# Optimization experiments

Measured on AMD Instinct MI355X. Metric: run time of the kernel, lower is better.

The kernel has to match this reference:

```python
import jax, jax.numpy as jnp
import numpy as np

D_MODEL = 512
N_HEADS = 8
D_HEAD = D_MODEL // N_HEADS


def setup_inputs() -> dict:
    key = jax.random.key(0)
    ks = jax.random.split(key, 10)
    B, N = 4, 2048
    s = 1.0 / np.sqrt(D_MODEL)
    inp = {
        'x': jax.random.normal(ks[0], (B, N, D_MODEL), jnp.float32),
        'attn_bias': jax.random.normal(ks[1], (B, 1, N, N), jnp.float32),
        'wq': jax.random.normal(ks[2], (D_MODEL, D_MODEL), jnp.float32) * s,
        'bq': jnp.zeros((D_MODEL,), jnp.float32),
        'wk': jax.random.normal(ks[3], (D_MODEL, D_MODEL), jnp.float32) * s,
        'bk': jnp.zeros((D_MODEL,), jnp.float32),
        'wv': jax.random.normal(ks[4], (D_MODEL, D_MODEL), jnp.float32) * s,
        'bv': jnp.zeros((D_MODEL,), jnp.float32),
        'wo': jax.random.normal(ks[5], (D_MODEL, D_MODEL), jnp.float32) * s,
        'bo': jnp.zeros((D_MODEL,), jnp.float32),
    }
    return inp


def reference(x, attn_bias, wq, bq, wk, bk, wv, bv, wo, bo):
    B, N, D = x.shape
    h, dh = N_HEADS, D_HEAD
    # projections; weights stored as (in, out) so y = x @ w + b
    q = (x @ wq + bq).reshape(B, N, h, dh).transpose(0, 2, 1, 3)  # (B,h,N,dh)
    k = (x @ wk + bk).reshape(B, N, h, dh).transpose(0, 2, 1, 3)
    v = (x @ wv + bv).reshape(B, N, h, dh).transpose(0, 2, 1, 3)
    scores = jnp.einsum('bhnd,bhmd->bhnm', q, k) / jnp.sqrt(jnp.float32(dh))
    scores = scores + attn_bias  # broadcast over heads
    attn = jax.nn.softmax(scores, axis=-1)
    out = jnp.einsum('bhnm,bhmd->bhnd', attn, v)
    out = out.transpose(0, 2, 1, 3).reshape(B, N, D)
    return out @ wo + bo
```

## Files before the change

### kernel.cpp

```cpp
#include <hip/hip_runtime.h>
#include <hip/hip_bf16.h>

typedef __bf16 bf16x8 __attribute__((ext_vector_type(8)));
typedef float f32x4 __attribute__((ext_vector_type(4)));
using u16 = unsigned short;
using u32 = unsigned int;

#define LDSS 72

__device__ __forceinline__ u16 f2bf(float f) {
  union { float f; u32 u; } v; v.f = f;
  u32 r = v.u + 0x7fffu + ((v.u >> 16) & 1u);
  return (u16)(r >> 16);
}

__device__ __forceinline__ u32 cvt_pk_bf16(float lo, float hi) {
  u32 r;
  asm("v_cvt_pk_bf16_f32 %0, %1, %2" : "=v"(r) : "v"(lo), "v"(hi));
  return r;
}

__global__ void cast_x_kernel(const float* __restrict__ x, u16* __restrict__ xb) {
  int i = (blockIdx.x * 256 + threadIdx.x) * 8;
  float4 f0 = *(const float4*)&x[i];
  float4 f1 = *(const float4*)&x[i + 4];
  u16 u[8];
  u[0] = f2bf(f0.x); u[1] = f2bf(f0.y); u[2] = f2bf(f0.z); u[3] = f2bf(f0.w);
  u[4] = f2bf(f1.x); u[5] = f2bf(f1.y); u[6] = f2bf(f1.z); u[7] = f2bf(f1.w);
  *(uint4*)&xb[i] = *(uint4*)u;
}

__global__ void cast_wT_kernel(const float* __restrict__ w0, const float* __restrict__ w1,
                               const float* __restrict__ w2, const float* __restrict__ w3,
                               u16* __restrict__ t0, u16* __restrict__ t1,
                               u16* __restrict__ t2, u16* __restrict__ t3) {
  int i = blockIdx.x * 256 + threadIdx.x;
  int wi = i >> 18;
  int r = i & 262143;
  int row = r >> 9, col = r & 511;
  const float* w; u16* t;
  if (wi == 0)      { w = w0; t = t0; }
  else if (wi == 1) { w = w1; t = t1; }
  else if (wi == 2) { w = w2; t = t2; }
  else              { w = w3; t = t3; }
  t[col * 512 + row] = f2bf(w[r]);
}

__global__ __launch_bounds__(256) void proj_kernel(
    const u16* __restrict__ xb,
    const u16* __restrict__ wqT, const u16* __restrict__ wkT, const u16* __restrict__ wvT,
    const float* __restrict__ bq, const float* __restrict__ bk, const float* __restrict__ bv,
    u16* __restrict__ Q, u16* __restrict__ K, u16* __restrict__ Vt) {
  __shared__ u16 Alds[64 * LDSS];
  __shared__ u16 Blds[64 * LDSS];
  int which = blockIdx.z;
  const u16* wT; const float* bias; u16* out;
  if (which == 0)      { wT = wqT; bias = bq; out = Q; }
  else if (which == 1) { wT = wkT; bias = bk; out = K; }
  else                 { wT = wvT; bias = bv; out = Vt; }

  int m0 = blockIdx.y * 64;
  int n0 = blockIdx.x * 64;
  int tid = threadIdx.x;
  int lane = tid & 63, w = tid >> 6;
  int wm = w >> 1, wn = w & 1;
  int l15 = lane & 15, l4 = lane >> 4;

  f32x4 acc[2][2] = {};
  for (int k0 = 0; k0 < 512; k0 += 64) {
    __syncthreads();
#pragma unroll
    for (int c = tid; c < 512; c += 256) {
      int row = c >> 3, c8 = (c & 7) * 8;
      *(uint4*)&Alds[row * LDSS + c8] = *(const uint4*)&xb[(m0 + row) * 512 + k0 + c8];
      *(uint4*)&Blds[row * LDSS + c8] = *(const uint4*)&wT[(n0 + row) * 512 + k0 + c8];
    }
    __syncthreads();
#pragma unroll
    for (int kk = 0; kk < 2; kk++) {
      bf16x8 a[2], b[2];
#pragma unroll
      for (int f = 0; f < 2; f++) {
        a[f] = *(const bf16x8*)&Alds[(wm * 32 + f * 16 + l15) * LDSS + kk * 32 + l4 * 8];
        b[f] = *(const bf16x8*)&Blds[(wn * 32 + f * 16 + l15) * LDSS + kk * 32 + l4 * 8];
      }
#pragma unroll
      for (int fm = 0; fm < 2; fm++)
#pragma unroll
        for (int fn = 0; fn < 2; fn++) {
          if (which == 2)
            acc[fm][fn] = __builtin_amdgcn_mfma_f32_16x16x32_bf16(b[fn], a[fm], acc[fm][fn], 0, 0, 0);
          else
            acc[fm][fn] = __builtin_amdgcn_mfma_f32_16x16x32_bf16(a[fm], b[fn], acc[fm][fn], 0, 0, 0);
        }
    }
  }
  int bidx = m0 >> 11;
  int head = n0 >> 6;
  if (which == 2) {
#pragma unroll
    for (int fm = 0; fm < 2; fm++)
#pragma unroll
      for (int fn = 0; fn < 2; fn++)
#pragma unroll
        for (int r = 0; r < 4; r++) {
          int drow = wn * 32 + fn * 16 + l4 * 4 + r;
          int col  = wm * 32 + fm * 16 + l15;
          float vv = acc[fm][fn][r] + bias[n0 + drow];
          out[((size_t)(bidx * 8 + head) * 64 + drow) * 2048 + (m0 & 2047) + col] = f2bf(vv);
        }
  } else {
#pragma unroll
    for (int fm = 0; fm < 2; fm++)
#pragma unroll
      for (int fn = 0; fn < 2; fn++)
#pragma unroll
        for (int r = 0; r < 4; r++) {
          int row = wm * 32 + fm * 16 + l4 * 4 + r;
          int col = wn * 32 + fn * 16 + l15;
          int nrow = (m0 & 2047) + row;
          float vv = acc[fm][fn][r] + bias[n0 + col];
          out[(((size_t)(bidx * 8 + head) * 2048) + nrow) * 64 + col] = f2bf(vv);
        }
  }
}

__global__ __launch_bounds__(512, 4) void attn_kernel(
    const u16* __restrict__ Q, const u16* __restrict__ K, const u16* __restrict__ Vt,
    const float* __restrict__ bias, u16* __restrict__ O) {
  __shared__ u16 Klds[64 * LDSS];
  __shared__ u16 Vtlds[64 * LDSS];

  int qt = blockIdx.x, h = blockIdx.y, b = blockIdx.z;
  int tid = threadIdx.x;
  int lane = tid & 63, w = tid >> 6;
  int l15 = lane & 15, l4 = lane >> 4;
  int qrow = qt * 128 + w * 16 + l15;

  const u16* Qbh  = Q  + (size_t)(b * 8 + h) * 2048 * 64;
  const u16* Kbh  = K  + (size_t)(b * 8 + h) * 2048 * 64;
  const u16* Vtbh = Vt + (size_t)(b * 8 + h) * 64 * 2048;
  const float* biasrow = bias + (size_t)b * 2048 * 2048 + (size_t)qrow * 2048;

  bf16x8 aq[2];
#pragma unroll
  for (int kk = 0; kk < 2; kk++)
    aq[kk] = *(const bf16x8*)&Qbh[qrow * 64 + kk * 32 + l4 * 8];

  f32x4 o[4] = {};
  float mrow = -1e30f, lrow = 0.f;

  int srcA = (lane & 16) * 2 + l15;
  bool hiF = (l4 >> 1) != 0;

  int srow = tid >> 3, sc8 = (tid & 7) * 8;

  uint4 kr = *(const uint4*)&Kbh[srow * 64 + sc8];
  uint4 vr = *(const uint4*)&Vtbh[srow * 2048 + sc8];
  float4 bb[4];
#pragma unroll
  for (int fj = 0; fj < 4; fj++)
    bb[fj] = *(const float4*)&biasrow[fj * 16 + l4 * 4];

  for (int t = 0; t < 32; t++) {
    __syncthreads();
    *(uint4*)&Klds[srow * LDSS + sc8]  = kr;
    *(uint4*)&Vtlds[srow * LDSS + sc8] = vr;
    __syncthreads();

    bool pf = (t < 31);
    float4 nbb[4];
    if (pf) {
      kr = *(const uint4*)&Kbh[((t + 1) * 64 + srow) * 64 + sc8];
      vr = *(const uint4*)&Vtbh[srow * 2048 + (t + 1) * 64 + sc8];
#pragma unroll
      for (int fj = 0; fj < 4; fj++)
        nbb[fj] = *(const float4*)&biasrow[(t + 1) * 64 + fj * 16 + l4 * 4];
    }

    f32x4 s[4] = {};
#pragma unroll
    for (int kk = 0; kk < 2; kk++)
#pragma unroll
      for (int fj = 0; fj < 4; fj++) {
        bf16x8 kf = *(const bf16x8*)&Klds[(fj * 16 + l15) * LDSS + kk * 32 + l4 * 8];
        s[fj] = __builtin_amdgcn_mfma_f32_16x16x32_bf16(kf, aq[kk], s[fj], 0, 0, 0);
      }

    float m = -1e30f;
#pragma unroll
    for (int fj = 0; fj < 4; fj++)
#pragma unroll
      for (int r = 0; r < 4; r++) {
        s[fj][r] = s[fj][r] * 0.125f + ((const float*)&bb[fj])[r];
        m = fmaxf(m, s[fj][r]);
      }
    m = fmaxf(m, __shfl_xor(m, 16));
    m = fmaxf(m, __shfl_xor(m, 32));
    float mnew = fmaxf(mrow, m);
    float corr = __expf(mrow - mnew);
    mrow = mnew;

    u32 pk[4][2];
    float sum = 0.f;
#pragma unroll
    for (int fj = 0; fj < 4; fj++) {
      float p0 = __expf(s[fj][0] - mnew);
      float p1 = __expf(s[fj][1] - mnew);
      float p2 = __expf(s[fj][2] - mnew);
      float p3 = __expf(s[fj][3] - mnew);
      sum += (p0 + p1) + (p2 + p3);
      pk[fj][0] = cvt_pk_bf16(p0, p1);
      pk[fj][1] = cvt_pk_bf16(p2, p3);
    }
    sum += __shfl_xor(sum, 16);
    sum += __shfl_xor(sum, 32);
    lrow = lrow * corr + sum;
#pragma unroll
    for (int fo = 0; fo < 4; fo++)
#pragma unroll
      for (int r = 0; r < 4; r++) o[fo][r] *= corr;

#pragma unroll
    for (int kk = 0; kk < 2; kk++) {
      u32 a0 = __shfl((int)pk[2 * kk][0],     srcA);
      u32 b0 = __shfl((int)pk[2 * kk + 1][0], srcA);
      u32 a1 = __shfl((int)pk[2 * kk][1],     srcA);
      u32 b1 = __shfl((int)pk[2 * kk + 1][1], srcA);
      u32 a2 = __shfl((int)pk[2 * kk][0],     srcA + 16);
      u32 b2 = __shfl((int)pk[2 * kk + 1][0], srcA + 16);
      u32 a3 = __shfl((int)pk[2 * kk][1],     srcA + 16);
      u32 b3 = __shfl((int)pk[2 * kk + 1][1], srcA + 16);
      union { u32 u[4]; bf16x8 v; } pu;
      pu.u[0] = hiF ? b0 : a0;
      pu.u[1] = hiF ? b1 : a1;
      pu.u[2] = hiF ? b2 : a2;
      pu.u[3] = hiF ? b3 : a3;
#pragma unroll
      for (int fo = 0; fo < 4; fo++) {
        bf16x8 vt = *(const bf16x8*)&Vtlds[(fo * 16 + l15) * LDSS + kk * 32 + l4 * 8];
        o[fo] = __builtin_amdgcn_mfma_f32_16x16x32_bf16(vt, pu.v, o[fo], 0, 0, 0);
      }
    }

    if (pf) {
#pragma unroll
      for (int fj = 0; fj < 4; fj++) bb[fj] = nbb[fj];
    }
  }

  float inv = 1.0f / lrow;
  size_t obase = (size_t)(b * 2048 + qrow) * 512 + h * 64;
#pragma unroll
  for (int fo = 0; fo < 4; fo++) {
    u32 wlo = cvt_pk_bf16(o[fo][0] * inv, o[fo][1] * inv);
    u32 whi = cvt_pk_bf16(o[fo][2] * inv, o[fo][3] * inv);
    *(u32*)&O[obase + fo * 16 + l4 * 4]     = wlo;
    *(u32*)&O[obase + fo * 16 + l4 * 4 + 2] = whi;
  }
}

__global__ __launch_bounds__(256) void outproj_kernel(
    const u16* __restrict__ Ob, const u16* __restrict__ woT,
    const float* __restrict__ bo, float* __restrict__ out) {
  __shared__ u16 Alds[64 * LDSS];
  __shared__ u16 Blds[64 * LDSS];
  int m0 = blockIdx.y * 64;
  int n0 = blockIdx.x * 64;
  int tid = threadIdx.x;
  int lane = tid & 63, w = tid >> 6;
  int wm = w >> 1, wn = w & 1;
  int l15 = lane & 15, l4 = lane >> 4;

  f32x4 acc[2][2] = {};
  for (int k0 = 0; k0 < 512; k0 += 64) {
    __syncthreads();
#pragma unroll
    for (int c = tid; c < 512; c += 256) {
      int row = c >> 3, c8 = (c & 7) * 8;
      *(uint4*)&Alds[row * LDSS + c8] = *(const uint4*)&Ob[(m0 + row) * 512 + k0 + c8];
      *(uint4*)&Blds[row * LDSS + c8] = *(const uint4*)&woT[(n0 + row) * 512 + k0 + c8];
    }
    __syncthreads();
#pragma unroll
    for (int kk = 0; kk < 2; kk++) {
      bf16x8 a[2], bfr[2];
#pragma unroll
      for (int f = 0; f < 2; f++) {
        a[f] = *(const bf16x8*)&Alds[(wm * 32 + f * 16 + l15) * LDSS + kk * 32 + l4 * 8];
        bfr[f] = *(const bf16x8*)&Blds[(wn * 32 + f * 16 + l15) * LDSS + kk * 32 + l4 * 8];
      }
#pragma unroll
      for (int fm = 0; fm < 2; fm++)
#pragma unroll
        for (int fn = 0; fn < 2; fn++)
          acc[fm][fn] = __builtin_amdgcn_mfma_f32_16x16x32_bf16(a[fm], bfr[fn], acc[fm][fn], 0, 0, 0);
    }
  }
#pragma unroll
  for (int fm = 0; fm < 2; fm++)
#pragma unroll
    for (int fn = 0; fn < 2; fn++)
#pragma unroll
      for (int r = 0; r < 4; r++) {
        int row = wm * 32 + fm * 16 + l4 * 4 + r;
        int col = wn * 32 + fn * 16 + l15;
        out[(size_t)(m0 + row) * 512 + n0 + col] = acc[fm][fn][r] + bo[n0 + col];
      }
}

extern "C" void kernel_launch(void* const* d_in, const int* in_sizes, int n_in,
                              void* d_out, int out_size, void* d_ws, size_t ws_size,
                              hipStream_t stream) {
  const float* x    = (const float*)d_in[0];
  const float* bias = (const float*)d_in[1];
  const float* wq   = (const float*)d_in[2];
  const float* bq   = (const float*)d_in[3];
  const float* wk   = (const float*)d_in[4];
  const float* bk   = (const float*)d_in[5];
  const float* wv   = (const float*)d_in[6];
  const float* bv   = (const float*)d_in[7];
  const float* wo   = (const float*)d_in[8];
  const float* bo   = (const float*)d_in[9];
  float* out = (float*)d_out;

  char* ws = (char*)d_ws;
  u16* xb  = (u16*)(ws + 0);
  u16* wqT = (u16*)(ws + 8388608);
  u16* wkT = (u16*)(ws + 8912896);
  u16* wvT = (u16*)(ws + 9437184);
  u16* woT = (u16*)(ws + 9961472);
  u16* Qb  = (u16*)(ws + 10485760);
  u16* Kb  = (u16*)(ws + 18874368);
  u16* VtB = (u16*)(ws + 27262976);
  u16* Ob  = (u16*)(ws + 35651584);

  hipLaunchKernelGGL(cast_x_kernel, dim3(2048), dim3(256), 0, stream, x, xb);
  hipLaunchKernelGGL(cast_wT_kernel, dim3(4096), dim3(256), 0, stream,
                     wq, wk, wv, wo, wqT, wkT, wvT, woT);
  hipLaunchKernelGGL(proj_kernel, dim3(8, 128, 3), dim3(256), 0, stream,
                     xb, wqT, wkT, wvT, bq, bk, bv, Qb, Kb, VtB);
  hipLaunchKernelGGL(attn_kernel, dim3(16, 8, 4), dim3(512), 0, stream,
                     Qb, Kb, VtB, bias, Ob);
  hipLaunchKernelGGL(outproj_kernel, dim3(8, 128), dim3(256), 0, stream,
                     Ob, woT, bo, out);
}
```

Measured before the change: 154.3 us.

## Prefetch GEMM tiles in registers, shrink attention blocks, add lazy rescale and setprio

The projection and output-projection GEMMs now load the next K-slice into registers while computing on the current LDS tile, which overlaps global loads with MFMA work. The attention kernel moves from 512-thread blocks covering 128 query rows to 256-thread blocks covering 64 rows, doubling the grid. It also adds s_setprio around the MFMA sections and skips the online-softmax rescale unless the running max grows by more than 8. The lazy rescale saves exp and multiply work per tile, but lets unnormalised exponentials reach up to e^8 before correction.

```diff
diff --git a/kernel.cpp b/kernel.cpp
--- a/kernel.cpp
+++ b/kernel.cpp
@@ -66,16 +66,28 @@
   int wm = w >> 1, wn = w & 1;
   int l15 = lane & 15, l4 = lane >> 4;
 
+  int r0 = tid >> 3, c8 = (tid & 7) * 8;
+
+  uint4 ar0 = *(const uint4*)&xb[(m0 + r0) * 512 + c8];
+  uint4 ar1 = *(const uint4*)&xb[(m0 + r0 + 32) * 512 + c8];
+  uint4 br0 = *(const uint4*)&wT[(n0 + r0) * 512 + c8];
+  uint4 br1 = *(const uint4*)&wT[(n0 + r0 + 32) * 512 + c8];
+
   f32x4 acc[2][2] = {};
-  for (int k0 = 0; k0 < 512; k0 += 64) {
-    __syncthreads();
-#pragma unroll
-    for (int c = tid; c < 512; c += 256) {
-      int row = c >> 3, c8 = (c & 7) * 8;
-      *(uint4*)&Alds[row * LDSS + c8] = *(const uint4*)&xb[(m0 + row) * 512 + k0 + c8];
-      *(uint4*)&Blds[row * LDSS + c8] = *(const uint4*)&wT[(n0 + row) * 512 + k0 + c8];
-    }
-    __syncthreads();
+  for (int ks = 0; ks < 8; ks++) {
+    __syncthreads();
+    *(uint4*)&Alds[r0 * LDSS + c8]        = ar0;
+    *(uint4*)&Alds[(r0 + 32) * LDSS + c8] = ar1;
+    *(uint4*)&Blds[r0 * LDSS + c8]        = br0;
+    *(uint4*)&Blds[(r0 + 32) * LDSS + c8] = br1;
+    __syncthreads();
+    if (ks < 7) {
+      int k0 = (ks + 1) * 64;
+      ar0 = *(const uint4*)&xb[(m0 + r0) * 512 + k0 + c8];
+      ar1 = *(const uint4*)&xb[(m0 + r0 + 32) * 512 + k0 + c8];
+      br0 = *(const uint4*)&wT[(n0 + r0) * 512 + k0 + c8];
+      br1 = *(const uint4*)&wT[(n0 + r0 + 32) * 512 + k0 + c8];
+    }
 #pragma unroll
     for (int kk = 0; kk < 2; kk++) {
       bf16x8 a[2], b[2];
@@ -125,7 +137,7 @@
   }
 }
 
-__global__ __launch_bounds__(512, 4) void attn_kernel(
+__global__ __launch_bounds__(256, 4) void attn_kernel(
     const u16* __restrict__ Q, const u16* __restrict__ K, const u16* __restrict__ Vt,
     const float* __restrict__ bias, u16* __restrict__ O) {
   __shared__ u16 Klds[64 * LDSS];
@@ -135,7 +147,7 @@
   int tid = threadIdx.x;
   int lane = tid & 63, w = tid >> 6;
   int l15 = lane & 15, l4 = lane >> 4;
-  int qrow = qt * 128 + w * 16 + l15;
+  int qrow = qt * 64 + w * 16 + l15;
 
   const u16* Qbh  = Q  + (size_t)(b * 8 + h) * 2048 * 64;
   const u16* Kbh  = K  + (size_t)(b * 8 + h) * 2048 * 64;
@@ -153,10 +165,12 @@
   int srcA = (lane & 16) * 2 + l15;
   bool hiF = (l4 >> 1) != 0;
 
-  int srow = tid >> 3, sc8 = (tid & 7) * 8;
-
-  uint4 kr = *(const uint4*)&Kbh[srow * 64 + sc8];
-  uint4 vr = *(const uint4*)&Vtbh[srow * 2048 + sc8];
+  int r0 = tid >> 3, c8 = (tid & 7) * 8;
+
+  uint4 kr0 = *(const uint4*)&Kbh[r0 * 64 + c8];
+  uint4 kr1 = *(const uint4*)&Kbh[(32 + r0) * 64 + c8];
+  uint4 vr0 = *(const uint4*)&Vtbh[r0 * 2048 + c8];
+  uint4 vr1 = *(const uint4*)&Vtbh[(r0 + 32) * 2048 + c8];
   float4 bb[4];
 #pragma unroll
   for (int fj = 0; fj < 4; fj++)
@@ -164,21 +178,26 @@
 
   for (int t = 0; t < 32; t++) {
     __syncthreads();
-    *(uint4*)&Klds[srow * LDSS + sc8]  = kr;
-    *(uint4*)&Vtlds[srow * LDSS + sc8] = vr;
+    *(uint4*)&Klds[r0 * LDSS + c8]         = kr0;
+    *(uint4*)&Klds[(r0 + 32) * LDSS + c8]  = kr1;
+    *(uint4*)&Vtlds[r0 * LDSS + c8]        = vr0;
+    *(uint4*)&Vtlds[(r0 + 32) * LDSS + c8] = vr1;
     __syncthreads();
 
     bool pf = (t < 31);
     float4 nbb[4];
     if (pf) {
-      kr = *(const uint4*)&Kbh[((t + 1) * 64 + srow) * 64 + sc8];
-      vr = *(const uint4*)&Vtbh[srow * 2048 + (t + 1) * 64 + sc8];
+      kr0 = *(const uint4*)&Kbh[((t + 1) * 64 + r0) * 64 + c8];
+      kr1 = *(const uint4*)&Kbh[((t + 1) * 64 + 32 + r0) * 64 + c8];
+      vr0 = *(const uint4*)&Vtbh[r0 * 2048 + (t + 1) * 64 + c8];
+      vr1 = *(const uint4*)&Vtbh[(r0 + 32) * 2048 + (t + 1) * 64 + c8];
 #pragma unroll
       for (int fj = 0; fj < 4; fj++)
         nbb[fj] = *(const float4*)&biasrow[(t + 1) * 64 + fj * 16 + l4 * 4];
     }
 
     f32x4 s[4] = {};
+    __builtin_amdgcn_s_setprio(1);
 #pragma unroll
     for (int kk = 0; kk < 2; kk++)
 #pragma unroll
@@ -186,6 +205,7 @@
         bf16x8 kf = *(const bf16x8*)&Klds[(fj * 16 + l15) * LDSS + kk * 32 + l4 * 8];
         s[fj] = __builtin_amdgcn_mfma_f32_16x16x32_bf16(kf, aq[kk], s[fj], 0, 0, 0);
       }
+    __builtin_amdgcn_s_setprio(0);
 
     float m = -1e30f;
 #pragma unroll
@@ -197,29 +217,33 @@
       }
     m = fmaxf(m, __shfl_xor(m, 16));
     m = fmaxf(m, __shfl_xor(m, 32));
-    float mnew = fmaxf(mrow, m);
-    float corr = __expf(mrow - mnew);
-    mrow = mnew;
+
+    if (!__all(m <= mrow + 8.0f)) {
+      float mnew = fmaxf(mrow, m);
+      float corr = __expf(mrow - mnew);
+      mrow = mnew;
+      lrow *= corr;
+#pragma unroll
+      for (int fo = 0; fo < 4; fo++)
+#pragma unroll
+        for (int r = 0; r < 4; r++) o[fo][r] *= corr;
+    }
 
     u32 pk[4][2];
     float sum = 0.f;
 #pragma unroll
     for (int fj = 0; fj < 4; fj++) {
-      float p0 = __expf(s[fj][0] - mnew);
-      float p1 = __expf(s[fj][1] - mnew);
-      float p2 = __expf(s[fj][2] - mnew);
-      float p3 = __expf(s[fj][3] - mnew);
+      float p0 = __expf(s[fj][0] - mrow);
+      float p1 = __expf(s[fj][1] - mrow);
+      float p2 = __expf(s[fj][2] - mrow);
+      float p3 = __expf(s[fj][3] - mrow);
       sum += (p0 + p1) + (p2 + p3);
       pk[fj][0] = cvt_pk_bf16(p0, p1);
       pk[fj][1] = cvt_pk_bf16(p2, p3);
     }
     sum += __shfl_xor(sum, 16);
     sum += __shfl_xor(sum, 32);
-    lrow = lrow * corr + sum;
-#pragma unroll
-    for (int fo = 0; fo < 4; fo++)
-#pragma unroll
-      for (int r = 0; r < 4; r++) o[fo][r] *= corr;
+    lrow += sum;
 
 #pragma unroll
     for (int kk = 0; kk < 2; kk++) {
@@ -236,11 +260,13 @@
       pu.u[1] = hiF ? b1 : a1;
       pu.u[2] = hiF ? b2 : a2;
       pu.u[3] = hiF ? b3 : a3;
+      __builtin_amdgcn_s_setprio(1);
 #pragma unroll
       for (int fo = 0; fo < 4; fo++) {
         bf16x8 vt = *(const bf16x8*)&Vtlds[(fo * 16 + l15) * LDSS + kk * 32 + l4 * 8];
         o[fo] = __builtin_amdgcn_mfma_f32_16x16x32_bf16(vt, pu.v, o[fo], 0, 0, 0);
       }
+      __builtin_amdgcn_s_setprio(0);
     }
 
     if (pf) {
@@ -272,16 +298,27 @@
   int wm = w >> 1, wn = w & 1;
   int l15 = lane & 15, l4 = lane >> 4;
 
+  int r0 = tid >> 3, c8 = (tid & 7) * 8;
+  uint4 ar0 = *(const uint4*)&Ob[(m0 + r0) * 512 + c8];
+  uint4 ar1 = *(const uint4*)&Ob[(m0 + r0 + 32) * 512 + c8];
+  uint4 br0 = *(const uint4*)&woT[(n0 + r0) * 512 + c8];
+  uint4 br1 = *(const uint4*)&woT[(n0 + r0 + 32) * 512 + c8];
+
   f32x4 acc[2][2] = {};
-  for (int k0 = 0; k0 < 512; k0 += 64) {
-    __syncthreads();
-#pragma unroll
-    for (int c = tid; c < 512; c += 256) {
-      int row = c >> 3, c8 = (c & 7) * 8;
-      *(uint4*)&Alds[row * LDSS + c8] = *(const uint4*)&Ob[(m0 + row) * 512 + k0 + c8];
-      *(uint4*)&Blds[row * LDSS + c8] = *(const uint4*)&woT[(n0 + row) * 512 + k0 + c8];
-    }
-    __syncthreads();
+  for (int ks = 0; ks < 8; ks++) {
+    __syncthreads();
+    *(uint4*)&Alds[r0 * LDSS + c8]        = ar0;
+    *(uint4*)&Alds[(r0 + 32) * LDSS + c8] = ar1;
+    *(uint4*)&Blds[r0 * LDSS + c8]        = br0;
+    *(uint4*)&Blds[(r0 + 32) * LDSS + c8] = br1;
+    __syncthreads();
+    if (ks < 7) {
+      int k0 = (ks + 1) * 64;
+      ar0 = *(const uint4*)&Ob[(m0 + r0) * 512 + k0 + c8];
+      ar1 = *(const uint4*)&Ob[(m0 + r0 + 32) * 512 + k0 + c8];
+      br0 = *(const uint4*)&woT[(n0 + r0) * 512 + k0 + c8];
+      br1 = *(const uint4*)&woT[(n0 + r0 + 32) * 512 + k0 + c8];
+    }
 #pragma unroll
     for (int kk = 0; kk < 2; kk++) {
       bf16x8 a[2], bfr[2];
@@ -340,7 +377,7 @@
                      wq, wk, wv, wo, wqT, wkT, wvT, woT);
   hipLaunchKernelGGL(proj_kernel, dim3(8, 128, 3), dim3(256), 0, stream,
                      xb, wqT, wkT, wvT, bq, bk, bv, Qb, Kb, VtB);
-  hipLaunchKernelGGL(attn_kernel, dim3(16, 8, 4), dim3(512), 0, stream,
+  hipLaunchKernelGGL(attn_kernel, dim3(32, 8, 4), dim3(256), 0, stream,
                      Qb, Kb, VtB, bias, Ob);
   hipLaunchKernelGGL(outproj_kernel, dim3(8, 128), dim3(256), 0, stream,
                      Ob, woT, bo, out);
```

Result: faster. 149.3 us (-3.2%).
